# Kernel optimization log

Hardware: AMD Instinct MI355X
Metric: run time of the kernel (lower is better)

Reference implementation:

```python
import jax, jax.numpy as jnp
import numpy as np

HEADS = 8
DIM_HEAD = 64
SCALE = DIM_HEAD ** -0.5
EPS = 1e-5


def layernorm(t, g, b):
    mu = t.mean(-1, keepdims=True)
    var = ((t - mu) ** 2).mean(-1, keepdims=True)
    return (t - mu) * jax.lax.rsqrt(var + EPS) * g + b


def setup_inputs() -> dict:
    key = jax.random.key(0)
    ks = jax.random.split(key, 12)
    b, n, dim, inner = 2, 2048, 512, HEADS * DIM_HEAD
    s = dim ** -0.5
    return {
        "x": jax.random.normal(ks[0], (b, n, dim), jnp.float32),
        "context": jax.random.normal(ks[1], (b, n, dim), jnp.float32),
        "g_x": jnp.ones((dim,), jnp.float32),
        "b_x": jnp.zeros((dim,), jnp.float32),
        "g_c": jnp.ones((dim,), jnp.float32),
        "b_c": jnp.zeros((dim,), jnp.float32),
        "W_qk": jax.random.normal(ks[2], (dim, inner), jnp.float32) * s,
        "W_cqk": jax.random.normal(ks[3], (dim, inner), jnp.float32) * s,
        "W_v": jax.random.normal(ks[4], (dim, inner), jnp.float32) * s,
        "W_cv": jax.random.normal(ks[5], (dim, inner), jnp.float32) * s,
        "W_out": jax.random.normal(ks[6], (inner, dim), jnp.float32) * s,
        "b_out": jnp.zeros((dim,), jnp.float32),
        "W_cout": jax.random.normal(ks[7], (inner, dim), jnp.float32) * s,
        "b_cout": jnp.zeros((dim,), jnp.float32),
    }


def reference(x, context, g_x, b_x, g_c, b_c, W_qk, W_cqk, W_v, W_cv, W_out, b_out, W_cout, b_cout):
    b, i, _ = x.shape
    j = context.shape[1]
    xn = layernorm(x, g_x, b_x)
    cn = layernorm(context, g_c, b_c)

    def split_heads(t):  # [b, n, h*d] -> [b, h, n, d]
        return t.reshape(t.shape[0], t.shape[1], HEADS, DIM_HEAD).transpose(0, 2, 1, 3)

    qk = split_heads(xn @ W_qk)
    cqk = split_heads(cn @ W_cqk)
    v = split_heads(xn @ W_v)
    cv = split_heads(cn @ W_cv)

    sim = jnp.einsum('bhid,bhjd->bhij', qk, cqk) * SCALE  # [b,h,i,j]
    attn = jax.nn.softmax(sim, axis=-1)           # rows: x attends to context
    context_attn = jax.nn.softmax(sim, axis=-2)   # cols: context attends to x

    out = jnp.einsum('bhij,bhjd->bhid', attn, cv)            # [b,h,i,d]
    context_out = jnp.einsum('bhij,bhid->bhjd', context_attn, v)  # [b,h,j,d]

    def merge_heads(t):  # [b,h,n,d] -> [b,n,h*d]
        return t.transpose(0, 2, 1, 3).reshape(t.shape[0], t.shape[2], HEADS * DIM_HEAD)

    out = merge_heads(out) @ W_out + b_out
    context_out = merge_heads(context_out) @ W_cout + b_cout
    return out, context_out
```

## Files before the change

### kernel.cpp

```cpp
#include <hip/hip_runtime.h>


typedef _Float16 half_t;
typedef __attribute__((ext_vector_type(2))) _Float16 half2v;
typedef __attribute__((ext_vector_type(4))) _Float16 half4v;
typedef __attribute__((ext_vector_type(8))) _Float16 half8v;
typedef __attribute__((ext_vector_type(4))) float floatx4;
typedef __attribute__((ext_vector_type(16))) float floatx16;

#define MFMA16(a, b, c) __builtin_amdgcn_mfma_f32_16x16x32_f16((a), (b), (c), 0, 0, 0)
#define MFMA32(a, b, c) __builtin_amdgcn_mfma_f32_32x32x16_f16((a), (b), (c), 0, 0, 0)

#if defined(__has_builtin)
#if __has_builtin(__builtin_amdgcn_exp2f)
#define EXP2F(x) __builtin_amdgcn_exp2f(x)
#else
#define EXP2F(x) exp2f(x)
#endif
#else
#define EXP2F(x) exp2f(x)
#endif

__device__ __forceinline__ half2v pk2(float a, float b) {
#if defined(__has_builtin) && __has_builtin(__builtin_amdgcn_cvt_pkrtz)
    union { __fp16 __attribute__((ext_vector_type(2))) i; half2v o; } u;
    u.i = __builtin_amdgcn_cvt_pkrtz(a, b);
    return u.o;
#else
    half2v r; r[0] = (half_t)a; r[1] = (half_t)b; return r;
#endif
}

__device__ __forceinline__ void gld16(const half_t* g, half_t* l) {
    __builtin_amdgcn_global_load_lds(
        (const __attribute__((address_space(1))) void*)g,
        (__attribute__((address_space(3))) void*)l, 16, 0, 0);
}

__global__ __launch_bounds__(256) void prep_kernel(
    const float* __restrict__ x, const float* __restrict__ ctx,
    const float* __restrict__ gx, const float* __restrict__ bx,
    const float* __restrict__ gc, const float* __restrict__ bc,
    half_t* __restrict__ xn, half_t* __restrict__ cn,
    const float* __restrict__ W0, const float* __restrict__ W1,
    const float* __restrict__ W2, const float* __restrict__ W3,
    const float* __restrict__ W4, const float* __restrict__ W5,
    half_t* __restrict__ Wt)
{
    __shared__ alignas(16) half_t Ts[128][136];
    const int blk = blockIdx.x;
    const int tid = threadIdx.x;
    const int wave = tid >> 6, lane = tid & 63;

    if (blk < 2048) {
        const int row = blk * 4 + wave;
        const float *src, *g, *b;
        half_t* dst;
        if (row < 4096) {
            src = x + (size_t)row * 512; g = gx; b = bx; dst = xn + (size_t)row * 512;
        } else {
            const size_t r = (size_t)(row - 4096);
            src = ctx + r * 512; g = gc; b = bc; dst = cn + r * 512;
        }
        const float4 a0 = *(const float4*)(src + lane * 4);
        const float4 a1 = *(const float4*)(src + 256 + lane * 4);
        float s = a0.x + a0.y + a0.z + a0.w + a1.x + a1.y + a1.z + a1.w;
        float q = a0.x * a0.x + a0.y * a0.y + a0.z * a0.z + a0.w * a0.w +
                  a1.x * a1.x + a1.y * a1.y + a1.z * a1.z + a1.w * a1.w;
#pragma unroll
        for (int m = 1; m < 64; m <<= 1) {
            s += __shfl_xor(s, m);
            q += __shfl_xor(q, m);
        }
        const float mean = s * (1.0f / 512.0f);
        const float var = q * (1.0f / 512.0f) - mean * mean;
        const float rs = rsqrtf(var + 1e-5f);
        const float4 g0 = *(const float4*)(g + lane * 4);
        const float4 g1 = *(const float4*)(g + 256 + lane * 4);
        const float4 b0 = *(const float4*)(b + lane * 4);
        const float4 b1 = *(const float4*)(b + 256 + lane * 4);
        half4v h0, h1;
        h0[0] = (half_t)((a0.x - mean) * rs * g0.x + b0.x);
        h0[1] = (half_t)((a0.y - mean) * rs * g0.y + b0.y);
        h0[2] = (half_t)((a0.z - mean) * rs * g0.z + b0.z);
        h0[3] = (half_t)((a0.w - mean) * rs * g0.w + b0.w);
        h1[0] = (half_t)((a1.x - mean) * rs * g1.x + b1.x);
        h1[1] = (half_t)((a1.y - mean) * rs * g1.y + b1.y);
        h1[2] = (half_t)((a1.z - mean) * rs * g1.z + b1.z);
        h1[3] = (half_t)((a1.w - mean) * rs * g1.w + b1.w);
        *(half4v*)(dst + lane * 4) = h0;
        *(half4v*)(dst + 256 + lane * 4) = h1;
        return;
    }

    const int b2 = blk - 2048;
    const int mat = b2 >> 4, tile = b2 & 15;
    const float* src;
    switch (mat) {
        case 0: src = W0; break;
        case 1: src = W1; break;
        case 2: src = W2; break;
        case 3: src = W3; break;
        case 4: src = W4; break;
        default: src = W5; break;
    }
    const int tr0 = (tile >> 2) * 128;
    const int tc0 = (tile & 3) * 128;
#pragma unroll
    for (int p = 0; p < 16; ++p) {
        const int idx = p * 256 + tid;
        const int r = idx >> 5, c4 = (idx & 31) * 4;
        const float4 w = *(const float4*)(src + (size_t)(tr0 + r) * 512 + tc0 + c4);
        Ts[c4 + 0][r] = (half_t)w.x;
        Ts[c4 + 1][r] = (half_t)w.y;
        Ts[c4 + 2][r] = (half_t)w.z;
        Ts[c4 + 3][r] = (half_t)w.w;
    }
    __syncthreads();
    half_t* dst = Wt + (size_t)mat * 262144;
#pragma unroll
    for (int p = 0; p < 8; ++p) {
        const int idx = p * 256 + tid;
        const int row = idx >> 4, ch = (idx & 15) * 8;
        *(half8v*)(dst + (size_t)(tc0 + row) * 512 + tr0 + ch) = *(const half8v*)&Ts[row][ch];
    }
}

__global__ __launch_bounds__(256) void gemm_in_kernel(
    const half_t* __restrict__ xn, const half_t* __restrict__ cn,
    const half_t* __restrict__ Wt,
    half_t* __restrict__ qk, half_t* __restrict__ v_t,
    half_t* __restrict__ cqk, half_t* __restrict__ cv_t)
{
    const half_t* A; const half_t* B; half_t* O;
    switch (blockIdx.z) {
        case 0:  A = xn; B = Wt;          O = qk;   break;
        case 1:  A = xn; B = Wt + 262144; O = v_t;  break;
        case 2:  A = cn; B = Wt + 524288; O = cqk;  break;
        default: A = cn; B = Wt + 786432; O = cv_t; break;
    }
    const int tr = blockIdx.z & 1;
    const int mt0 = blockIdx.x * 128;
    const int nt0 = blockIdx.y * 128;

    __shared__ alignas(16) half_t As[128 * 64];
    __shared__ alignas(16) half_t Ws[128 * 64];

    const int tid = threadIdx.x;
    const int wave = tid >> 6, lane = tid & 63;
    const int wr = wave >> 1, wc = wave & 1;
    const int q4 = lane >> 4, c = lane & 15;

    int srow[4], scol[4];
#pragma unroll
    for (int p = 0; p < 4; ++p) {
        const int ofs = p * 4096 + wave * 1024 + lane * 16;
        const int row = ofs >> 7;
        const int pc = (ofs >> 4) & 7;
        srow[p] = row;
        scol[p] = (pc ^ (row & 7)) * 8;
    }

    const half_t* P1 = tr ? As : Ws;
    const half_t* P2 = tr ? Ws : As;

    const floatx4 z4 = {0.f, 0.f, 0.f, 0.f};
    floatx4 acc[4][4];
#pragma unroll
    for (int mt = 0; mt < 4; ++mt)
#pragma unroll
        for (int nt = 0; nt < 4; ++nt) acc[mt][nt] = z4;

    for (int kb = 0; kb < 8; ++kb) {
        const int k0 = kb * 64;
#pragma unroll
        for (int p = 0; p < 4; ++p) {
            const int lofs = p * 2048 + wave * 512;
            gld16(A + (size_t)(mt0 + srow[p]) * 512 + k0 + scol[p], As + lofs);
            gld16(B + (size_t)(nt0 + srow[p]) * 512 + k0 + scol[p], Ws + lofs);
        }
        __syncthreads();
#pragma unroll
        for (int kt = 0; kt < 2; ++kt) {
            half8v f1[4], f2[4];
#pragma unroll
            for (int i = 0; i < 4; ++i) {
                const int r1 = wr * 64 + i * 16 + c;
                const int r2 = wc * 64 + i * 16 + c;
                f1[i] = *(const half8v*)&P1[(r1 << 6) + (((kt * 4 + q4) ^ (r1 & 7)) << 3)];
                f2[i] = *(const half8v*)&P2[(r2 << 6) + (((kt * 4 + q4) ^ (r2 & 7)) << 3)];
            }
#pragma unroll
            for (int mt = 0; mt < 4; ++mt)
#pragma unroll
                for (int nt = 0; nt < 4; ++nt)
                    acc[mt][nt] = MFMA16(f1[mt], f2[nt], acc[mt][nt]);
        }
        __syncthreads();
    }

    const int bb = mt0 >> 11;
    const int nnb = mt0 & 2047;
    if (tr) {
#pragma unroll
        for (int mt = 0; mt < 4; ++mt) {
            const int row = nnb + wr * 64 + mt * 16 + q4 * 4;
#pragma unroll
            for (int nt = 0; nt < 4; ++nt) {
                const int col = nt0 + wc * 64 + nt * 16 + c;
                const int h = col >> 6, dd = col & 63;
                half4v pk;
                pk[0] = (half_t)acc[mt][nt][0];
                pk[1] = (half_t)acc[mt][nt][1];
                pk[2] = (half_t)acc[mt][nt][2];
                pk[3] = (half_t)acc[mt][nt][3];
                *(half4v*)(O + ((size_t)(bb * 8 + h) * 64 + dd) * 2048 + row) = pk;
            }
        }
    } else {
#pragma unroll
        for (int mt = 0; mt < 4; ++mt) {
            const int colw = nt0 + wr * 64 + mt * 16 + q4 * 4;
            const int h = colw >> 6, dd = colw & 63;
#pragma unroll
            for (int nt = 0; nt < 4; ++nt) {
                const int row = nnb + wc * 64 + nt * 16 + c;
                half4v pk;
                pk[0] = (half_t)acc[mt][nt][0];
                pk[1] = (half_t)acc[mt][nt][1];
                pk[2] = (half_t)acc[mt][nt][2];
                pk[3] = (half_t)acc[mt][nt][3];
                *(half4v*)(O + ((size_t)(bb * 8 + h) * 2048 + row) * 64 + dd) = pk;
            }
        }
    }
}

__device__ __forceinline__ void stage_tile64(const half_t* Kt, const half_t* Vt,
                                             half_t* ksb, half_t* cvb,
                                             int wave, int lane)
{
#pragma unroll
    for (int p = 0; p < 2; ++p) {
        const int base = p * 256 + wave * 64;
        const int cidx = base + lane;
        const int R = cidx >> 3, ch = cidx & 7;
        const int gR = (R & ~12) | ((R & 4) << 1) | ((R & 8) >> 1);
        const int ksw = ((R >> 2) ^ (R & 3)) & 7;
        gld16(Kt + (size_t)gR * 64 + ((ch ^ ksw) * 8), ksb + base * 8);
        gld16(Vt + (size_t)R * 2048 + ((ch ^ (R & 7)) * 8), cvb + base * 8);
    }
}

__global__ __launch_bounds__(256, 4) void flash_kernel(
    const half_t* __restrict__ qk, const half_t* __restrict__ cqk,
    const half_t* __restrict__ v_t, const half_t* __restrict__ cv_t,
    float* __restrict__ Pbuf, float* __restrict__ Lbuf)
{
    const int bh = blockIdx.x, it = blockIdx.y;
    const int dir = blockIdx.z >> 1, js = blockIdx.z & 1;
    const half_t* Q  = dir ? cqk : qk;
    const half_t* K  = dir ? qk  : cqk;
    const half_t* VT = dir ? v_t : cv_t;
    const half_t* Qb = Q + (size_t)bh * (2048 * 64);
    const half_t* Kb = K + (size_t)bh * (2048 * 64);
    const half_t* VTb = VT + (size_t)bh * (64 * 2048);
    float* Pb = Pbuf + (size_t)((js * 2 + dir) * 16 + bh) * (2048 * 64);
    float* Lb = Lbuf + (size_t)((js * 2 + dir) * 16 + bh) * 2048;

    __shared__ alignas(16) half_t Ks[2][64 * 64];
    __shared__ alignas(16) half_t CVs[2][64 * 64];

    const int tid = threadIdx.x;
    const int wave = tid >> 6, lane = tid & 63;
    const int h = lane >> 5, i5 = lane & 31;

    half8v qf[4];
#pragma unroll
    for (int ks = 0; ks < 4; ++ks) {
        half8v v = *(const half8v*)(Qb +
            (size_t)(it * 128 + wave * 32 + i5) * 64 + ks * 16 + h * 8);
        qf[ks] = v * (half_t)0.18033688f;
    }

    floatx16 accO[2];
    float accL = 0.f;
#pragma unroll
    for (int dt = 0; dt < 2; ++dt)
#pragma unroll
        for (int q = 0; q < 16; ++q) accO[dt][q] = 0.f;

    const int jt0 = js * 16;
    stage_tile64(Kb + (size_t)jt0 * 4096, VTb + jt0 * 64, Ks[0], CVs[0], wave, lane);
    __syncthreads();

    const int swk = ((i5 >> 2) ^ (i5 & 3)) & 7;
    const int swv = i5 & 7;

    for (int n = 0; n < 16; ++n) {
        const int jt = jt0 + n;
        const int cur = n & 1;
        if (n < 15)
            stage_tile64(Kb + (size_t)(jt + 1) * 4096, VTb + (size_t)(jt + 1) * 64,
                         Ks[cur ^ 1], CVs[cur ^ 1], wave, lane);
        const half_t* ksld = Ks[cur];
        const half_t* cvld = CVs[cur];

#pragma unroll
        for (int g = 0; g < 2; ++g) {
            const int ksbase = (g * 32 + i5) * 64;
            half8v ka[4];
#pragma unroll
            for (int ks = 0; ks < 4; ++ks)
                ka[ks] = *(const half8v*)&ksld[ksbase + (((ks * 2 + h) ^ swk) << 3)];
            floatx16 st;
#pragma unroll
            for (int q = 0; q < 16; ++q) st[q] = 0.f;
            __builtin_amdgcn_s_setprio(1);
            st = MFMA32(ka[0], qf[0], st);
            st = MFMA32(ka[1], qf[1], st);
            st = MFMA32(ka[2], qf[2], st);
            st = MFMA32(ka[3], qf[3], st);
            __builtin_amdgcn_s_setprio(0);
            half8v pf[2];
            float lsum = 0.f;
#pragma unroll
            for (int s = 0; s < 2; ++s) {
                float ex[8];
#pragma unroll
                for (int e = 0; e < 8; ++e) {
                    ex[e] = EXP2F(fminf(st[8 * s + e], 15.0f));
                    lsum += ex[e];
                }
                union { half8v v; half2v h2[4]; } u;
                u.h2[0] = pk2(ex[0], ex[1]);
                u.h2[1] = pk2(ex[2], ex[3]);
                u.h2[2] = pk2(ex[4], ex[5]);
                u.h2[3] = pk2(ex[6], ex[7]);
                pf[s] = u.v;
            }
            accL += lsum;
            __builtin_amdgcn_s_setprio(1);
#pragma unroll
            for (int dt = 0; dt < 2; ++dt) {
                const int cvbase = (dt * 32 + i5) * 64;
#pragma unroll
                for (int s = 0; s < 2; ++s) {
                    const half8v cva = *(const half8v*)&cvld[cvbase +
                        (((g * 4 + s * 2 + h) ^ swv) << 3)];
                    accO[dt] = MFMA32(cva, pf[s], accO[dt]);
                }
            }
            __builtin_amdgcn_s_setprio(0);
        }
        __syncthreads();
    }

    {
        float l = accL;
        l += __shfl_xor(l, 32);
        const int i = it * 128 + wave * 32 + i5;
        if (h == 0) Lb[i] = l;
#pragma unroll
        for (int dt = 0; dt < 2; ++dt)
#pragma unroll
            for (int rq = 0; rq < 4; ++rq) {
                float4 o;
                o.x = accO[dt][4 * rq + 0];
                o.y = accO[dt][4 * rq + 1];
                o.z = accO[dt][4 * rq + 2];
                o.w = accO[dt][4 * rq + 3];
                *(float4*)(Pb + (size_t)i * 64 + dt * 32 + 8 * rq + 4 * h) = o;
            }
    }
}

__global__ __launch_bounds__(256) void combine_kernel(
    const float* __restrict__ Pbuf, const float* __restrict__ Lbuf,
    half_t* __restrict__ out_h, half_t* __restrict__ ctx_out_h)
{
    const int tid = threadIdx.x;
    const int rg = blockIdx.x * 16 + (tid >> 4);
    const int q = tid & 15;
    const int i = rg & 2047;
    const int bh = (rg >> 11) & 15;
    const int dir = rg >> 15;

    const size_t pb0 = (size_t)(dir * 16 + bh) * (2048 * 64) + (size_t)i * 64 + q * 4;
    const size_t pb1 = pb0 + (size_t)2 * 16 * 2048 * 64;
    const float4 a0 = *(const float4*)(Pbuf + pb0);
    const float4 a1 = *(const float4*)(Pbuf + pb1);
    const size_t lb0 = (size_t)(dir * 16 + bh) * 2048 + i;
    const float l = Lbuf[lb0] + Lbuf[lb0 + (size_t)2 * 16 * 2048];
    const float rl = 1.0f / l;

    half_t* Out = dir ? ctx_out_h : out_h;
    half4v pk;
    pk[0] = (half_t)((a0.x + a1.x) * rl);
    pk[1] = (half_t)((a0.y + a1.y) * rl);
    pk[2] = (half_t)((a0.z + a1.z) * rl);
    pk[3] = (half_t)((a0.w + a1.w) * rl);
    *(half4v*)(Out + (size_t)(bh >> 3) * 2048 * 512 + (size_t)i * 512 +
               (bh & 7) * 64 + q * 4) = pk;
}

__global__ __launch_bounds__(256) void gemm_out_kernel(
    const half_t* __restrict__ out_h, const half_t* __restrict__ ctx_out_h,
    const half_t* __restrict__ Wt,
    const float* __restrict__ bout, const float* __restrict__ bcout,
    float* __restrict__ dout)
{
    const half_t* A; const half_t* B; const float* bias; float* O;
    if (blockIdx.z == 0) { A = out_h;     B = Wt + 1048576; bias = bout;  O = dout; }
    else                 { A = ctx_out_h; B = Wt + 1310720; bias = bcout; O = dout + 2097152; }

    const int mt0 = blockIdx.x * 64;
    const int nt0 = blockIdx.y * 128;

    __shared__ alignas(16) half_t As[64 * 64];
    __shared__ alignas(16) half_t Ws[128 * 64];

    const int tid = threadIdx.x;
    const int wave = tid >> 6, lane = tid & 63;
    const int wr = wave >> 1, wc = wave & 1;
    const int q4 = lane >> 4, c = lane & 15;

    int srow[4], scol[4];
#pragma unroll
    for (int p = 0; p < 4; ++p) {
        const int ofs = p * 4096 + wave * 1024 + lane * 16;
        const int row = ofs >> 7;
        const int pc = (ofs >> 4) & 7;
        srow[p] = row;
        scol[p] = (pc ^ (row & 7)) * 8;
    }

    const floatx4 z4 = {0.f, 0.f, 0.f, 0.f};
    floatx4 acc[4][2];
#pragma unroll
    for (int mt = 0; mt < 4; ++mt)
#pragma unroll
        for (int nt = 0; nt < 2; ++nt) acc[mt][nt] = z4;

    for (int kb = 0; kb < 8; ++kb) {
        const int k0 = kb * 64;
#pragma unroll
        for (int p = 0; p < 4; ++p) {
            const int lofs = p * 2048 + wave * 512;
            gld16(B + (size_t)(nt0 + srow[p]) * 512 + k0 + scol[p], Ws + lofs);
            if (p < 2)
                gld16(A + (size_t)(mt0 + srow[p]) * 512 + k0 + scol[p], As + lofs);
        }
        __syncthreads();
#pragma unroll
        for (int kt = 0; kt < 2; ++kt) {
            half8v f1[4], f2[2];
#pragma unroll
            for (int i = 0; i < 4; ++i) {
                const int r1 = wr * 64 + i * 16 + c;
                f1[i] = *(const half8v*)&Ws[(r1 << 6) + (((kt * 4 + q4) ^ (r1 & 7)) << 3)];
            }
#pragma unroll
            for (int i = 0; i < 2; ++i) {
                const int r2 = wc * 32 + i * 16 + c;
                f2[i] = *(const half8v*)&As[(r2 << 6) + (((kt * 4 + q4) ^ (r2 & 7)) << 3)];
            }
#pragma unroll
            for (int mt = 0; mt < 4; ++mt)
#pragma unroll
                for (int nt = 0; nt < 2; ++nt)
                    acc[mt][nt] = MFMA16(f1[mt], f2[nt], acc[mt][nt]);
        }
        __syncthreads();
    }

#pragma unroll
    for (int mt = 0; mt < 4; ++mt) {
        const int col = nt0 + wr * 64 + mt * 16 + q4 * 4;
        const float4 bv = *(const float4*)(bias + col);
#pragma unroll
        for (int nt = 0; nt < 2; ++nt) {
            const int row = mt0 + wc * 32 + nt * 16 + c;
            float4 o;
            o.x = acc[mt][nt][0] + bv.x;
            o.y = acc[mt][nt][1] + bv.y;
            o.z = acc[mt][nt][2] + bv.z;
            o.w = acc[mt][nt][3] + bv.w;
            *(float4*)(O + (size_t)row * 512 + col) = o;
        }
    }
}

extern "C" void kernel_launch(void* const* d_in, const int* in_sizes, int n_in,
                              void* d_out, int out_size, void* d_ws, size_t ws_size,
                              hipStream_t stream)
{
    (void)in_sizes; (void)n_in; (void)out_size; (void)ws_size;
    const float* x      = (const float*)d_in[0];
    const float* ctx    = (const float*)d_in[1];
    const float* g_x    = (const float*)d_in[2];
    const float* b_x    = (const float*)d_in[3];
    const float* g_c    = (const float*)d_in[4];
    const float* b_c    = (const float*)d_in[5];
    const float* W_qk   = (const float*)d_in[6];
    const float* W_cqk  = (const float*)d_in[7];
    const float* W_v    = (const float*)d_in[8];
    const float* W_cv   = (const float*)d_in[9];
    const float* W_out  = (const float*)d_in[10];
    const float* b_out  = (const float*)d_in[11];
    const float* W_cout = (const float*)d_in[12];
    const float* b_cout = (const float*)d_in[13];
    float* out = (float*)d_out;

    half_t* ws = (half_t*)d_ws;
    const size_t SEG = 2097152;
    half_t* xn        = ws;
    half_t* cn        = ws + 1 * SEG;
    half_t* qk        = ws + 2 * SEG;
    half_t* cqk       = ws + 3 * SEG;
    half_t* v_t       = ws + 4 * SEG;
    half_t* cv_t      = ws + 5 * SEG;
    half_t* Wt        = ws + 6 * SEG;
    half_t* out_h     = xn;
    half_t* ctx_out_h = cn;
    float* Pbuf = (float*)(ws + 6 * SEG + 1572864);
    float* Lbuf = Pbuf + (size_t)2 * 2 * 16 * 2048 * 64;

    prep_kernel<<<2144, 256, 0, stream>>>(x, ctx, g_x, b_x, g_c, b_c, xn, cn,
                                          W_qk, W_v, W_cqk, W_cv, W_out, W_cout, Wt);
    gemm_in_kernel<<<dim3(32, 4, 4), 256, 0, stream>>>(xn, cn, Wt, qk, v_t, cqk, cv_t);
    flash_kernel<<<dim3(16, 16, 4), 256, 0, stream>>>(qk, cqk, v_t, cv_t, Pbuf, Lbuf);
    combine_kernel<<<4096, 256, 0, stream>>>(Pbuf, Lbuf, out_h, ctx_out_h);
    gemm_out_kernel<<<dim3(64, 4, 2), 256, 0, stream>>>(out_h, ctx_out_h, Wt, b_out, b_cout, out);
}
```

Measured before the change: 184.9 us.

## Fuse split-K combine into output GEMM and restructure flash inner loop

Removes the separate combine kernel: the output GEMM now reads the two fp32 partial accumulators and row sums, normalizes them, converts to half and writes the swizzled A tile into LDS itself. This drops one launch and the fp16 intermediate round trip, but each output GEMM block re-reads fp32 partials once per column tile (4 column blocks). The flash kernel's inner loop is manually unrolled so the second K-group fragment loads are issued while the first group's softmax and PV MMAs proceed. The row-sum accumulation now uses fdot2 on the packed half exponents, and K staging switches to a simpler XOR swizzle.

New measurement: 182.3 us. About the same (-1.4%).

```diff
diff --git a/kernel.cpp b/kernel.cpp
--- a/kernel.cpp
+++ b/kernel.cpp
@@ -16,6 +16,9 @@
 #define EXP2F(x) __builtin_amdgcn_exp2f(x)
 #else
 #define EXP2F(x) exp2f(x)
+#endif
+#if __has_builtin(__builtin_amdgcn_fdot2)
+#define HAS_FDOT2 1
 #endif
 #else
 #define EXP2F(x) exp2f(x)
@@ -246,8 +249,7 @@
         const int cidx = base + lane;
         const int R = cidx >> 3, ch = cidx & 7;
         const int gR = (R & ~12) | ((R & 4) << 1) | ((R & 8) >> 1);
-        const int ksw = ((R >> 2) ^ (R & 3)) & 7;
-        gld16(Kt + (size_t)gR * 64 + ((ch ^ ksw) * 8), ksb + base * 8);
+        gld16(Kt + (size_t)gR * 64 + ((ch ^ (R & 7)) * 8), ksb + base * 8);
         gld16(Vt + (size_t)R * 2048 + ((ch ^ (R & 7)) * 8), cvb + base * 8);
     }
 }
@@ -290,12 +292,13 @@
 #pragma unroll
         for (int q = 0; q < 16; ++q) accO[dt][q] = 0.f;
 
+    half2v one2; one2[0] = (half_t)1.0f; one2[1] = (half_t)1.0f;
+
     const int jt0 = js * 16;
     stage_tile64(Kb + (size_t)jt0 * 4096, VTb + jt0 * 64, Ks[0], CVs[0], wave, lane);
     __syncthreads();
 
-    const int swk = ((i5 >> 2) ^ (i5 & 3)) & 7;
-    const int swv = i5 & 7;
+    const int swk = i5 & 7;
 
     for (int n = 0; n < 16; ++n) {
         const int jt = jt0 + n;
@@ -306,53 +309,100 @@
         const half_t* ksld = Ks[cur];
         const half_t* cvld = CVs[cur];
 
-#pragma unroll
-        for (int g = 0; g < 2; ++g) {
-            const int ksbase = (g * 32 + i5) * 64;
-            half8v ka[4];
-#pragma unroll
-            for (int ks = 0; ks < 4; ++ks)
-                ka[ks] = *(const half8v*)&ksld[ksbase + (((ks * 2 + h) ^ swk) << 3)];
-            floatx16 st;
-#pragma unroll
-            for (int q = 0; q < 16; ++q) st[q] = 0.f;
-            __builtin_amdgcn_s_setprio(1);
-            st = MFMA32(ka[0], qf[0], st);
-            st = MFMA32(ka[1], qf[1], st);
-            st = MFMA32(ka[2], qf[2], st);
-            st = MFMA32(ka[3], qf[3], st);
-            __builtin_amdgcn_s_setprio(0);
-            half8v pf[2];
-            float lsum = 0.f;
+        half8v ka0[4], ka1[4];
+#pragma unroll
+        for (int ks = 0; ks < 4; ++ks)
+            ka0[ks] = *(const half8v*)&ksld[i5 * 64 + (((ks * 2 + h) ^ swk) << 3)];
+        floatx16 st;
+#pragma unroll
+        for (int q = 0; q < 16; ++q) st[q] = 0.f;
+        __builtin_amdgcn_s_setprio(1);
+        st = MFMA32(ka0[0], qf[0], st);
+        st = MFMA32(ka0[1], qf[1], st);
+        st = MFMA32(ka0[2], qf[2], st);
+        st = MFMA32(ka0[3], qf[3], st);
+        __builtin_amdgcn_s_setprio(0);
+#pragma unroll
+        for (int ks = 0; ks < 4; ++ks)
+            ka1[ks] = *(const half8v*)&ksld[(32 + i5) * 64 + (((ks * 2 + h) ^ swk) << 3)];
+
+        half8v pf[2];
+#pragma unroll
+        for (int s = 0; s < 2; ++s) {
+            float ex[8];
+#pragma unroll
+            for (int e = 0; e < 8; ++e)
+                ex[e] = EXP2F(fminf(st[8 * s + e], 15.0f));
+            union { half8v v; half2v h2[4]; } u;
+            u.h2[0] = pk2(ex[0], ex[1]);
+            u.h2[1] = pk2(ex[2], ex[3]);
+            u.h2[2] = pk2(ex[4], ex[5]);
+            u.h2[3] = pk2(ex[6], ex[7]);
+            pf[s] = u.v;
+#ifdef HAS_FDOT2
+#pragma unroll
+            for (int t2 = 0; t2 < 4; ++t2)
+                accL = __builtin_amdgcn_fdot2(u.h2[t2], one2, accL, false);
+#else
+#pragma unroll
+            for (int e = 0; e < 8; ++e) accL += ex[e];
+#endif
+        }
+        __builtin_amdgcn_s_setprio(1);
+#pragma unroll
+        for (int dt = 0; dt < 2; ++dt) {
+            const int cvbase = (dt * 32 + i5) * 64;
 #pragma unroll
             for (int s = 0; s < 2; ++s) {
-                float ex[8];
-#pragma unroll
-                for (int e = 0; e < 8; ++e) {
-                    ex[e] = EXP2F(fminf(st[8 * s + e], 15.0f));
-                    lsum += ex[e];
-                }
-                union { half8v v; half2v h2[4]; } u;
-                u.h2[0] = pk2(ex[0], ex[1]);
-                u.h2[1] = pk2(ex[2], ex[3]);
-                u.h2[2] = pk2(ex[4], ex[5]);
-                u.h2[3] = pk2(ex[6], ex[7]);
-                pf[s] = u.v;
-            }
-            accL += lsum;
-            __builtin_amdgcn_s_setprio(1);
-#pragma unroll
-            for (int dt = 0; dt < 2; ++dt) {
-                const int cvbase = (dt * 32 + i5) * 64;
-#pragma unroll
-                for (int s = 0; s < 2; ++s) {
-                    const half8v cva = *(const half8v*)&cvld[cvbase +
-                        (((g * 4 + s * 2 + h) ^ swv) << 3)];
-                    accO[dt] = MFMA32(cva, pf[s], accO[dt]);
-                }
-            }
-            __builtin_amdgcn_s_setprio(0);
-        }
+                const half8v cva = *(const half8v*)&cvld[cvbase +
+                    (((s * 2 + h) ^ swk) << 3)];
+                accO[dt] = MFMA32(cva, pf[s], accO[dt]);
+            }
+        }
+        __builtin_amdgcn_s_setprio(0);
+
+#pragma unroll
+        for (int q = 0; q < 16; ++q) st[q] = 0.f;
+        __builtin_amdgcn_s_setprio(1);
+        st = MFMA32(ka1[0], qf[0], st);
+        st = MFMA32(ka1[1], qf[1], st);
+        st = MFMA32(ka1[2], qf[2], st);
+        st = MFMA32(ka1[3], qf[3], st);
+        __builtin_amdgcn_s_setprio(0);
+#pragma unroll
+        for (int s = 0; s < 2; ++s) {
+            float ex[8];
+#pragma unroll
+            for (int e = 0; e < 8; ++e)
+                ex[e] = EXP2F(fminf(st[8 * s + e], 15.0f));
+            union { half8v v; half2v h2[4]; } u;
+            u.h2[0] = pk2(ex[0], ex[1]);
+            u.h2[1] = pk2(ex[2], ex[3]);
+            u.h2[2] = pk2(ex[4], ex[5]);
+            u.h2[3] = pk2(ex[6], ex[7]);
+            pf[s] = u.v;
+#ifdef HAS_FDOT2
+#pragma unroll
+            for (int t2 = 0; t2 < 4; ++t2)
+                accL = __builtin_amdgcn_fdot2(u.h2[t2], one2, accL, false);
+#else
+#pragma unroll
+            for (int e = 0; e < 8; ++e) accL += ex[e];
+#endif
+        }
+        __builtin_amdgcn_s_setprio(1);
+#pragma unroll
+        for (int dt = 0; dt < 2; ++dt) {
+            const int cvbase = (dt * 32 + i5) * 64;
+#pragma unroll
+            for (int s = 0; s < 2; ++s) {
+                const half8v cva = *(const half8v*)&cvld[cvbase +
+                    (((4 + s * 2 + h) ^ swk) << 3)];
+                accO[dt] = MFMA32(cva, pf[s], accO[dt]);
+            }
+        }
+        __builtin_amdgcn_s_setprio(0);
+
         __syncthreads();
     }
 
@@ -375,44 +425,16 @@
     }
 }
 
-__global__ __launch_bounds__(256) void combine_kernel(
+__global__ __launch_bounds__(256) void gemm_out_kernel(
     const float* __restrict__ Pbuf, const float* __restrict__ Lbuf,
-    half_t* __restrict__ out_h, half_t* __restrict__ ctx_out_h)
-{
-    const int tid = threadIdx.x;
-    const int rg = blockIdx.x * 16 + (tid >> 4);
-    const int q = tid & 15;
-    const int i = rg & 2047;
-    const int bh = (rg >> 11) & 15;
-    const int dir = rg >> 15;
-
-    const size_t pb0 = (size_t)(dir * 16 + bh) * (2048 * 64) + (size_t)i * 64 + q * 4;
-    const size_t pb1 = pb0 + (size_t)2 * 16 * 2048 * 64;
-    const float4 a0 = *(const float4*)(Pbuf + pb0);
-    const float4 a1 = *(const float4*)(Pbuf + pb1);
-    const size_t lb0 = (size_t)(dir * 16 + bh) * 2048 + i;
-    const float l = Lbuf[lb0] + Lbuf[lb0 + (size_t)2 * 16 * 2048];
-    const float rl = 1.0f / l;
-
-    half_t* Out = dir ? ctx_out_h : out_h;
-    half4v pk;
-    pk[0] = (half_t)((a0.x + a1.x) * rl);
-    pk[1] = (half_t)((a0.y + a1.y) * rl);
-    pk[2] = (half_t)((a0.z + a1.z) * rl);
-    pk[3] = (half_t)((a0.w + a1.w) * rl);
-    *(half4v*)(Out + (size_t)(bh >> 3) * 2048 * 512 + (size_t)i * 512 +
-               (bh & 7) * 64 + q * 4) = pk;
-}
-
-__global__ __launch_bounds__(256) void gemm_out_kernel(
-    const half_t* __restrict__ out_h, const half_t* __restrict__ ctx_out_h,
     const half_t* __restrict__ Wt,
     const float* __restrict__ bout, const float* __restrict__ bcout,
     float* __restrict__ dout)
 {
-    const half_t* A; const half_t* B; const float* bias; float* O;
-    if (blockIdx.z == 0) { A = out_h;     B = Wt + 1048576; bias = bout;  O = dout; }
-    else                 { A = ctx_out_h; B = Wt + 1310720; bias = bcout; O = dout + 2097152; }
+    const half_t* B; const float* bias; float* O;
+    const int dir = blockIdx.z;
+    if (dir == 0) { B = Wt + 1048576; bias = bout;  O = dout; }
+    else          { B = Wt + 1310720; bias = bcout; O = dout + 2097152; }
 
     const int mt0 = blockIdx.x * 64;
     const int nt0 = blockIdx.y * 128;
@@ -435,6 +457,9 @@
         scol[p] = (pc ^ (row & 7)) * 8;
     }
 
+    const size_t JSP = (size_t)2 * 16 * 2048 * 64;
+    const size_t JSL = (size_t)2 * 16 * 2048;
+
     const floatx4 z4 = {0.f, 0.f, 0.f, 0.f};
     floatx4 acc[4][2];
 #pragma unroll
@@ -448,8 +473,27 @@
         for (int p = 0; p < 4; ++p) {
             const int lofs = p * 2048 + wave * 512;
             gld16(B + (size_t)(nt0 + srow[p]) * 512 + k0 + scol[p], Ws + lofs);
-            if (p < 2)
-                gld16(A + (size_t)(mt0 + srow[p]) * 512 + k0 + scol[p], As + lofs);
+        }
+#pragma unroll
+        for (int p = 0; p < 2; ++p) {
+            const int cidx = p * 256 + tid;
+            const int R = cidx >> 3, ch = cidx & 7;
+            const int r = mt0 + R;
+            const int b = r >> 11, i = r & 2047;
+            const size_t base = (size_t)(dir * 16 + b * 8 + kb) * (2048 * 64) +
+                                (size_t)i * 64 + ch * 8;
+            const float4 a0 = *(const float4*)(Pbuf + base);
+            const float4 a1 = *(const float4*)(Pbuf + base + 4);
+            const float4 c0 = *(const float4*)(Pbuf + base + JSP);
+            const float4 c1 = *(const float4*)(Pbuf + base + 4 + JSP);
+            const size_t lb = (size_t)(dir * 16 + b * 8 + kb) * 2048 + i;
+            const float rl = 1.0f / (Lbuf[lb] + Lbuf[lb + JSL]);
+            union { half8v v; half2v h2[4]; } u;
+            u.h2[0] = pk2((a0.x + c0.x) * rl, (a0.y + c0.y) * rl);
+            u.h2[1] = pk2((a0.z + c0.z) * rl, (a0.w + c0.w) * rl);
+            u.h2[2] = pk2((a1.x + c1.x) * rl, (a1.y + c1.y) * rl);
+            u.h2[3] = pk2((a1.z + c1.z) * rl, (a1.w + c1.w) * rl);
+            *(half8v*)&As[R * 64 + ((ch ^ (R & 7)) * 8)] = u.v;
         }
         __syncthreads();
 #pragma unroll
@@ -521,8 +565,6 @@
     half_t* v_t       = ws + 4 * SEG;
     half_t* cv_t      = ws + 5 * SEG;
     half_t* Wt        = ws + 6 * SEG;
-    half_t* out_h     = xn;
-    half_t* ctx_out_h = cn;
     float* Pbuf = (float*)(ws + 6 * SEG + 1572864);
     float* Lbuf = Pbuf + (size_t)2 * 2 * 16 * 2048 * 64;
 
@@ -530,6 +572,5 @@
                                           W_qk, W_v, W_cqk, W_cv, W_out, W_cout, Wt);
     gemm_in_kernel<<<dim3(32, 4, 4), 256, 0, stream>>>(xn, cn, Wt, qk, v_t, cqk, cv_t);
     flash_kernel<<<dim3(16, 16, 4), 256, 0, stream>>>(qk, cqk, v_t, cv_t, Pbuf, Lbuf);
-    combine_kernel<<<4096, 256, 0, stream>>>(Pbuf, Lbuf, out_h, ctx_out_h);
-    gemm_out_kernel<<<dim3(64, 4, 2), 256, 0, stream>>>(out_h, ctx_out_h, Wt, b_out, b_cout, out);
-}
+    gemm_out_kernel<<<dim3(64, 4, 2), 256, 0, stream>>>(Pbuf, Lbuf, Wt, b_out, b_cout, out);
+}
```
